# Kernel optimization log

Hardware: AMD Instinct MI355X
Metric: run time of the kernel (lower is better)

The kernel has to match this reference:

```python
import jax, jax.numpy as jnp
import numpy as np

N = 20000
E = 640000
F_IN = 128
C_T = 8
L_T = 10 * N
HEADS = 8
HDIM = 64
NEG_SLOPE = 0.2


def setup_inputs() -> dict:
    key = jax.random.key(0)
    ks = jax.random.split(key, 20)
    d = {}
    d["x"] = jax.random.normal(ks[0], (N, F_IN), dtype=jnp.float32)
    d["edge_index"] = jax.random.randint(ks[1], (2, E), 0, N, dtype=jnp.int64)
    d["temporal"] = jax.random.normal(ks[2], (C_T, L_T), dtype=jnp.float32)
    # GCNConv(F_IN, 16)
    d["W1"] = jax.random.normal(ks[3], (F_IN, 16), dtype=jnp.float32) * 0.1
    d["b1"] = jnp.zeros((16,), dtype=jnp.float32)
    # GATConv(16, 64, heads=8), concat -> 512
    d["W2"] = jax.random.normal(ks[4], (16, HEADS * HDIM), dtype=jnp.float32) * 0.1
    d["att_src"] = jax.random.normal(ks[5], (HEADS, HDIM), dtype=jnp.float32) * 0.1
    d["att_dst"] = jax.random.normal(ks[6], (HEADS, HDIM), dtype=jnp.float32) * 0.1
    d["b2"] = jnp.zeros((HEADS * HDIM,), dtype=jnp.float32)
    # TemporalCNN
    d["cw1"] = jax.random.normal(ks[7], (32, C_T, 3), dtype=jnp.float32) * 0.1
    d["cb1"] = jnp.zeros((32,), dtype=jnp.float32)
    d["cw2"] = jax.random.normal(ks[8], (64, 32, 3), dtype=jnp.float32) * 0.05
    d["cb2"] = jnp.zeros((64,), dtype=jnp.float32)
    d["cw3"] = jax.random.normal(ks[9], (128, 64, 3), dtype=jnp.float32) * 0.05
    d["cb3"] = jnp.zeros((128,), dtype=jnp.float32)
    d["fw1"] = jax.random.normal(ks[10], (256, 128 * 10), dtype=jnp.float32) * 0.02
    d["fb1"] = jnp.zeros((256,), dtype=jnp.float32)
    d["fw2"] = jax.random.normal(ks[11], (64, 256), dtype=jnp.float32) * 0.05
    d["fb2"] = jnp.zeros((64,), dtype=jnp.float32)
    return d


def _conv1d(x, w, b):
    # x: [1, C, L], w: [O, C, 3]; padding=1 == SAME for k=3
    out = jax.lax.conv_general_dilated(
        x, w, window_strides=(1,), padding="SAME",
        dimension_numbers=("NCH", "OIH", "NCH"))
    return out + b[None, :, None]


def _gcn(x, src, dst, W, b):
    # PyG GCNConv: add self-loops, symmetric normalization
    h = x @ W                                   # [N, 16]
    deg = jax.ops.segment_sum(jnp.ones_like(dst, dtype=h.dtype), dst, num_segments=N)
    dinv = jax.lax.rsqrt(jnp.maximum(deg, 1.0))
    norm = dinv[src] * dinv[dst]                # [E+N]
    out = jax.ops.segment_sum(h[src] * norm[:, None], dst, num_segments=N)
    return out + b


def _gat(x, src, dst, W, att_src, att_dst, b):
    h = (x @ W).reshape(N, HEADS, HDIM)         # [N, 8, 64]
    a_s = jnp.einsum("nhd,hd->nh", h, att_src)  # [N, 8]
    a_d = jnp.einsum("nhd,hd->nh", h, att_dst)
    e = a_s[src] + a_d[dst]                     # [E+N, 8], message j->i: src=j, dst=i
    e = jnp.where(e >= 0, e, NEG_SLOPE * e)     # LeakyReLU(0.2)
    # segment softmax over incoming edges of each dst node
    m = jax.ops.segment_max(e, dst, num_segments=N)
    m = jnp.where(jnp.isfinite(m), m, 0.0)
    ex = jnp.exp(e - m[dst])
    s = jax.ops.segment_sum(ex, dst, num_segments=N)
    alpha = ex / (s[dst] + 1e-16)               # [E+N, 8]
    out = jax.ops.segment_sum(h[src] * alpha[:, :, None], dst, num_segments=N)
    return out.reshape(N, HEADS * HDIM) + b


def reference(x, edge_index, temporal, W1, b1, W2, att_src, att_dst, b2,
              cw1, cb1, cw2, cb2, cw3, cb3, fw1, fb1, fw2, fb2):
    # ---- graph branch ----
    loops = jnp.arange(N, dtype=edge_index.dtype)
    src = jnp.concatenate([edge_index[0], loops])
    dst = jnp.concatenate([edge_index[1], loops])
    g = _gcn(x, src, dst, W1, b1)
    g = jax.nn.relu(g)
    # F.dropout with training=False (eval) -> identity
    x1 = _gat(g, src, dst, W2, att_src, att_dst, b2)   # [N, 512]
    # ---- temporal branch ----
    t = temporal[None]                                  # [1, C, L]
    t = jax.nn.relu(_conv1d(t, cw1, cb1))
    t = jax.nn.relu(_conv1d(t, cw2, cb2))
    t = jax.nn.relu(_conv1d(t, cw3, cb3))               # [1, 128, L]
    t = t.reshape(-1, 128 * 10)                         # [N, 1280] (same as torch .view)
    t = jax.nn.relu(t @ fw1.T + fb1)
    x2 = t @ fw2.T + fb2                                # [N, 64]
    return jnp.concatenate([x1, x2], axis=1)            # [N, 576]
```

## Files before the change

### kernel.cpp

```cpp
#include <hip/hip_runtime.h>
#include <hip/hip_bf16.h>

#define NN 20000
#define EE 640000
#define FIN 128
#define CT 8
#define LT 200000
#define HEADS 8
#define HDIM 64
#define F1 16
#define F2 512
#define OUTF 576

typedef short s16x8 __attribute__((ext_vector_type(8)));
typedef float f32x4 __attribute__((ext_vector_type(4)));
typedef float f32x2 __attribute__((ext_vector_type(2)));

static __device__ __forceinline__ float b2f(__hip_bfloat16 v) { return __bfloat162float(v); }
static __device__ __forceinline__ float ldf(float v) { return v; }
static __device__ __forceinline__ float ldf(__hip_bfloat16 v) { return __bfloat162float(v); }
static __device__ __forceinline__ unsigned f2bf_bits(float x) {
  unsigned u = __float_as_uint(x);
  return (u + 0x7fffu + ((u >> 16) & 1u)) >> 16;
}

static __device__ __forceinline__ void gl16(const void* g, void* l) {
  __builtin_amdgcn_global_load_lds(
      (const __attribute__((address_space(1))) unsigned*)g,
      (__attribute__((address_space(3))) unsigned*)l, 16, 0, 0);
}


__global__ __launch_bounds__(256) void wprep_kernel(
    const float* __restrict__ cw, float* __restrict__ wt, int O, int C) {
  int i = blockIdx.x * 256 + threadIdx.x;
  if (i >= O * C * 3) return;
  int o = i / (C * 3), r = i % (C * 3);
  int c = r / 3, k = r % 3;
  wt[(c * 3 + k) * O + o] = cw[i];
}

__global__ __launch_bounds__(256) void wprep_bf(
    const float* __restrict__ cw, short* __restrict__ wb, int O, int C) {
  int i = blockIdx.x * 256 + threadIdx.x;
  if (i >= O * C * 3) return;
  int o = i / (C * 3), r = i % (C * 3);
  int ic = r / 3, kk = r % 3;
  wb[o * 3 * C + kk * C + ic] = (short)f2bf_bits(cw[i]);
}

template <int C, int O, int P, typename IN_T>
__global__ __launch_bounds__(256) void conv_fast(
    const IN_T* __restrict__ in, __hip_bfloat16* __restrict__ out,
    const float* __restrict__ wt, const float* __restrict__ bias) {
  constexpr int OCG = O / 2;
  constexpr int PG = 256 / OCG;
  static_assert(PG * P == 64, "tile mismatch");
  __shared__ __align__(16) float tile[C][68];
  __shared__ __align__(16) __hip_bfloat16 ot[O][66];
  int t = threadIdx.x;
  int ocg = t % OCG;
  int pg = t / OCG;
  long base = (long)blockIdx.x * 64;

  for (int i = t; i < C * 66; i += 256) {
    int c = i / 66, p = i % 66;
    long l = base + p - 1;
    tile[c][p] = (l >= 0 && l < LT) ? ldf(in[(long)c * LT + l]) : 0.f;
  }
  __syncthreads();

  int oc0 = 2 * ocg;
  int p0 = pg * P;
  float acc[2][P];
#pragma unroll
  for (int j = 0; j < 2; j++)
#pragma unroll
    for (int p = 0; p < P; p++) acc[j][p] = 0.f;

  for (int ic = 0; ic < C; ic++) {
    float x[P + 2];
#pragma unroll
    for (int q = 0; q < P / 4; q++) {
      float4 v = *(const float4*)&tile[ic][p0 + 4 * q];
      x[4 * q] = v.x; x[4 * q + 1] = v.y; x[4 * q + 2] = v.z; x[4 * q + 3] = v.w;
    }
    {
      float2 v = *(const float2*)&tile[ic][p0 + P];
      x[P] = v.x; x[P + 1] = v.y;
    }
    const float* wrow = wt + (long)ic * 3 * O;
    float wv[3][2];
#pragma unroll
    for (int kk = 0; kk < 3; kk++) {
      float2 w2 = *(const float2*)&wrow[kk * O + oc0];
      wv[kk][0] = w2.x; wv[kk][1] = w2.y;
    }
#pragma unroll
    for (int kk = 0; kk < 3; kk++)
#pragma unroll
      for (int j = 0; j < 2; j++)
#pragma unroll
        for (int p = 0; p < P; p++) acc[j][p] += x[p + kk] * wv[kk][j];
  }
  float b0 = bias[oc0], b1 = bias[oc0 + 1];
#pragma unroll
  for (int p = 0; p < P; p++) {
    ot[oc0][p0 + p] = __float2bfloat16(fmaxf(acc[0][p] + b0, 0.f));
    ot[oc0 + 1][p0 + p] = __float2bfloat16(fmaxf(acc[1][p] + b1, 0.f));
  }
  __syncthreads();
  for (int i = t; i < O * 32; i += 256) {
    int oc = i >> 5, pp = i & 31;
    unsigned v = ((const unsigned*)&ot[oc][0])[pp];
    *(unsigned*)&out[(long)oc * LT + base + 2 * pp] = v;
  }
}

template <int C, int O, int MPW>
__global__ __launch_bounds__(256) void conv_mfma(
    const short* __restrict__ in, short* __restrict__ out,
    const short* __restrict__ w, const float* __restrict__ bias) {
  constexpr int K = 3 * C;
  constexpr int NS = K / 32;
  constexpr int XP = C + 8;
  constexpr int OP = 132;
  constexpr int SH_X = 132 * XP * 2;
  constexpr int SH_O = O * OP * 2;
  __shared__ __align__(16) char smem[(SH_X > SH_O) ? SH_X : SH_O];
  short* xT = (short*)smem;

  int t = threadIdx.x;
  long base = (long)blockIdx.x * 128;

  for (int idx = t; idx < C * 132; idx += 256) {
    int ic = idx / 132, p = idx % 132;
    long l = base + p - 1;
    xT[p * XP + ic] = (l >= 0 && l < LT) ? in[(long)ic * LT + l] : (short)0;
  }
  __syncthreads();

  int wave = t >> 6, lane = t & 63;
  int n = lane & 15, kg = lane >> 4;
  int m0 = wave * (MPW * 16);

  f32x4 acc[MPW][8] = {};
#pragma unroll
  for (int s = 0; s < NS; s++) {
    const int kk = (s * 32) / C;
    const int ic0 = (s * 32) % C + kg * 8;
    s16x8 a[MPW];
#pragma unroll
    for (int mi = 0; mi < MPW; mi++)
      a[mi] = *(const s16x8*)(w + (long)(m0 + mi * 16 + n) * K + s * 32 + kg * 8);
#pragma unroll
    for (int nt = 0; nt < 8; nt++) {
      s16x8 b = *(const s16x8*)(xT + (nt * 16 + n + kk) * XP + ic0);
#pragma unroll
      for (int mi = 0; mi < MPW; mi++)
        acc[mi][nt] = __builtin_amdgcn_mfma_f32_16x16x32_bf16(a[mi], b, acc[mi][nt], 0, 0, 0);
    }
  }

  __syncthreads();
  short* ob = (short*)smem;
#pragma unroll
  for (int mi = 0; mi < MPW; mi++) {
    int o = m0 + mi * 16 + kg * 4;
#pragma unroll
    for (int nt = 0; nt < 8; nt++) {
      int p = nt * 16 + n;
#pragma unroll
      for (int r = 0; r < 4; r++) {
        float v = fmaxf(acc[mi][nt][r] + bias[o + r], 0.f);
        ob[(o + r) * OP + p] = (short)f2bf_bits(v);
      }
    }
  }
  __syncthreads();
  const unsigned* obu = (const unsigned*)smem;
  for (int idx = t; idx < O * 64; idx += 256) {
    int o = idx >> 6, q = idx & 63;
    long l = base + 2 * q;
    if (l < LT)
      *(unsigned*)(out + (long)o * LT + l) = obu[o * (OP / 2) + q];
  }
}

__global__ __launch_bounds__(256) void fw1bf_kernel(
    const float* __restrict__ fw1, __hip_bfloat16* __restrict__ w) {
  int i = blockIdx.x * 256 + threadIdx.x;
  if (i < 256 * 1280) w[i] = __float2bfloat16(fw1[i]);
}

__global__ __launch_bounds__(256) void fw2t_kernel(
    const float* __restrict__ fw2, float* __restrict__ fw2t) {
  int i = blockIdx.x * 256 + threadIdx.x;
  if (i >= 64 * 256) return;
  int o = i / 256, j = i % 256;
  fw2t[j * 64 + o] = fw2[i];
}

__global__ __launch_bounds__(256) void fc1_tile(
    const __hip_bfloat16* __restrict__ t3, const __hip_bfloat16* __restrict__ w,
    const float* __restrict__ fb1, float* __restrict__ out) {
  __shared__ __align__(16) short As[2][128 * 32];
  __shared__ __align__(16) short Bs[2][128 * 32];
  int t = threadIdx.x;
  int wid = t >> 6, lane = t & 63;
  int bn = blockIdx.x & 1, bm = blockIdx.x >> 1;
  int mrow = lane & 15, kg = lane >> 4;

  const char* tb = (const char*)t3;
  const char* wb = (const char*)w;
  int u0 = wid * 128 + lane;
  int u1 = u0 + 64;
  int ra0 = u0 >> 2, ca0 = u0 & 3;
  int ra1 = u1 >> 2, ca1 = u1 & 3;
  long ga0 = ((long)min(bm * 128 + ra0, NN - 1) * 1280 + ca0 * 8) * 2;
  long ga1 = ((long)min(bm * 128 + ra1, NN - 1) * 1280 + ca1 * 8) * 2;
  long gb0 = ((long)(bn * 128 + ra0) * 1280 + ca0 * 8) * 2;
  long gb1 = ((long)(bn * 128 + ra1) * 1280 + ca1 * 8) * 2;
  int l0 = (wid * 2 + 0) * 512;
  int l1 = (wid * 2 + 1) * 512;

#define FC1_STAGE(buf, k0)                          \
  do {                                              \
    long kb = (long)(k0) * 2;                       \
    gl16(tb + ga0 + kb, &As[buf][l0]);              \
    gl16(tb + ga1 + kb, &As[buf][l1]);              \
    gl16(wb + gb0 + kb, &Bs[buf][l0]);              \
    gl16(wb + gb1 + kb, &Bs[buf][l1]);              \
  } while (0)

  FC1_STAGE(0, 0);
  __syncthreads();

  int wr = wid >> 1, wc = wid & 1;
  f32x4 acc[4][4] = {};
  for (int s = 0; s < 40; s++) {
    int buf = s & 1;
    if (s + 1 < 40) FC1_STAGE(buf ^ 1, (s + 1) * 32);
    s16x8 a[4], b[4];
#pragma unroll
    for (int mi = 0; mi < 4; mi++)
      a[mi] = *(const s16x8*)&As[buf][(wr * 64 + mi * 16 + mrow) * 32 + kg * 8];
#pragma unroll
    for (int ni = 0; ni < 4; ni++)
      b[ni] = *(const s16x8*)&Bs[buf][(wc * 64 + ni * 16 + mrow) * 32 + kg * 8];
#pragma unroll
    for (int mi = 0; mi < 4; mi++)
#pragma unroll
      for (int ni = 0; ni < 4; ni++)
        acc[mi][ni] = __builtin_amdgcn_mfma_f32_16x16x32_bf16(a[mi], b[ni], acc[mi][ni], 0, 0, 0);
    __syncthreads();
  }
#undef FC1_STAGE

  int node_base = bm * 128 + wr * 64 + kg * 4;
  int col_base = bn * 128 + wc * 64 + mrow;
#pragma unroll
  for (int ni = 0; ni < 4; ni++) {
    int col = col_base + ni * 16;
    float bias = fb1[col];
#pragma unroll
    for (int mi = 0; mi < 4; mi++) {
      int node = node_base + mi * 16;
#pragma unroll
      for (int r = 0; r < 4; r++) {
        if (node + r < NN)
          out[(long)(node + r) * 256 + col] = fmaxf(acc[mi][ni][r] + bias, 0.f);
      }
    }
  }
}

__global__ __launch_bounds__(256) void fc2_kernel(
    const float* __restrict__ fc1o, const float* __restrict__ fw2t,
    const float* __restrict__ fb2, float* __restrict__ out) {
  __shared__ float sh[32][257];
  int t = threadIdx.x;
  int m0 = blockIdx.x * 32;
  for (int i = t; i < 32 * 256; i += 256) {
    int nd = i >> 8, j = i & 255;
    sh[nd][j] = fc1o[(long)(m0 + nd) * 256 + j];
  }
  __syncthreads();
  int wave = t >> 6, o = t & 63;
  int nb = wave * 8;
  float acc[8];
  float bias = fb2[o];
#pragma unroll
  for (int i = 0; i < 8; i++) acc[i] = bias;
  for (int j = 0; j < 256; j++) {
    float wv = fw2t[j * 64 + o];
#pragma unroll
    for (int i = 0; i < 8; i++) acc[i] += sh[nb + i][j] * wv;
  }
#pragma unroll
  for (int i = 0; i < 8; i++)
    out[(long)(m0 + nb + i) * OUTF + F2 + o] = acc[i];
}


__global__ __launch_bounds__(256) void zero_i32(int* __restrict__ p, int n) {
  int i = blockIdx.x * 256 + threadIdx.x;
  if (i < n) p[i] = 0;
}

__global__ __launch_bounds__(256) void deg_kernel(const int* __restrict__ dst, int* __restrict__ deg) {
  int e = blockIdx.x * 256 + threadIdx.x;
  if (e < EE) atomicAdd(&deg[dst[e]], 1);
}

__global__ __launch_bounds__(256) void dinv_kernel(const int* __restrict__ deg, float* __restrict__ dinv) {
  int i = blockIdx.x * 256 + threadIdx.x;
  if (i < NN) dinv[i] = rsqrtf((float)(deg[i] + 1));
}

__global__ __launch_bounds__(1024) void scan_kernel(const int* __restrict__ deg, int* __restrict__ offs) {
  __shared__ int sums[1024];
  int tid = threadIdx.x;
  const int CH = 20;
  int s = 0;
  for (int i = 0; i < CH; i++) {
    int idx = tid * CH + i;
    if (idx < NN) s += deg[idx] + 1;
  }
  sums[tid] = s;
  __syncthreads();
  for (int off = 1; off < 1024; off <<= 1) {
    int v = (tid >= off) ? sums[tid - off] : 0;
    __syncthreads();
    sums[tid] += v;
    __syncthreads();
  }
  int run = (tid > 0) ? sums[tid - 1] : 0;
  for (int i = 0; i < CH; i++) {
    int idx = tid * CH + i;
    if (idx < NN) {
      offs[idx] = run;
      run += deg[idx] + 1;
    }
  }
  if (tid == 1023) offs[NN] = sums[1023];
}

__global__ __launch_bounds__(256) void fill_kernel(
    const int* __restrict__ src, const int* __restrict__ dst,
    const int* __restrict__ offs, int* __restrict__ cursor, int* __restrict__ csr) {
  int e = blockIdx.x * 256 + threadIdx.x;
  if (e < EE) {
    int d = dst[e];
    int pos = atomicAdd(&cursor[d], 1);
    csr[offs[d] + pos] = src[e];
  } else if (e < EE + NN) {
    int i = e - EE;
    int pos = atomicAdd(&cursor[i], 1);
    csr[offs[i] + pos] = i;
  }
}

__global__ __launch_bounds__(256) void h1_kernel(
    const float* __restrict__ x, const float* __restrict__ W1,
    const float* __restrict__ dinv, float* __restrict__ h1s) {
  __shared__ __align__(16) float ws[128 * 16];
  __shared__ __align__(16) float xs[16][132];
  int t = threadIdx.x;
  int i0 = blockIdx.x * 16;
#pragma unroll
  for (int i = t; i < 512; i += 256)
    *(float4*)&ws[4 * i] = *(const float4*)&W1[4 * i];
#pragma unroll
  for (int i = t; i < 512; i += 256) {
    int nl = i >> 5, q = i & 31;
    *(float4*)&xs[nl][4 * q] = *(const float4*)&x[(long)(i0 + nl) * FIN + 4 * q];
  }
  __syncthreads();
  int nl = t >> 4, f = t & 15;
  float acc = 0.f;
#pragma unroll 8
  for (int k = 0; k < FIN; k++) acc += xs[nl][k] * ws[k * 16 + f];
  int n = i0 + nl;
  h1s[n * F1 + f] = acc * dinv[n];
}

__global__ __launch_bounds__(256) void gcn_kernel(
    const float* __restrict__ h1s, const int* __restrict__ offs, const int* __restrict__ csr,
    const float* __restrict__ dinv, const float* __restrict__ b1, float* __restrict__ g) {
  int wave = threadIdx.x >> 6;
  int lane = threadIdx.x & 63;
  int i = blockIdx.x * 4 + wave;
  int f = lane & 15, grp = lane >> 4;
  int beg = offs[i], end = offs[i + 1];
  float acc = 0.f;
  for (int idx = beg + grp; idx < end; idx += 4)
    acc += h1s[csr[idx] * F1 + f];
  acc += __shfl_down(acc, 32);
  acc += __shfl_down(acc, 16);
  if (lane < 16) g[i * F1 + f] = fmaxf(acc * dinv[i] + b1[f], 0.f);
}

__global__ __launch_bounds__(256) void att_prep(
    const float* __restrict__ W2, const float* __restrict__ asrc,
    const float* __restrict__ adst, float* __restrict__ WS, float* __restrict__ WD) {
  int t = threadIdx.x;
  int k = (t & 127) >> 3, h = t & 7;
  const float* av = (t < 128) ? asrc : adst;
  float acc = 0.f;
  for (int d = 0; d < 64; d++) acc += W2[k * F2 + h * 64 + d] * av[h * 64 + d];
  ((t < 128) ? WS : WD)[k * 8 + h] = acc;
}

__global__ __launch_bounds__(256) void h2att_kernel(
    const float* __restrict__ g, const float* __restrict__ W2,
    const float* __restrict__ WS, const float* __restrict__ WD,
    unsigned* __restrict__ h2hm, float* __restrict__ AS, float* __restrict__ AD) {
  __shared__ __align__(16) float gl[32][20];
  int t = threadIdx.x;
  int i0 = blockIdx.x * 32;
  for (int idx = t; idx < 512; idx += 256)
    gl[idx >> 4][idx & 15] = g[i0 * 16 + idx];
  __syncthreads();

  int f0 = 2 * t;
  int h = t >> 5, c32 = t & 31;
  float w0[16], w1[16];
#pragma unroll
  for (int k = 0; k < 16; k++) {
    float2 wv = *(const float2*)&W2[k * F2 + f0];
    w0[k] = wv.x; w1[k] = wv.y;
  }
  for (int nl = 0; nl < 32; nl++) {
    float a0 = 0.f, a1 = 0.f;
#pragma unroll
    for (int kk = 0; kk < 4; kk++) {
      f32x4 gv = *(const f32x4*)&gl[nl][4 * kk];
#pragma unroll
      for (int r = 0; r < 4; r++) {
        a0 += gv[r] * w0[4 * kk + r];
        a1 += gv[r] * w1[4 * kk + r];
      }
    }
    h2hm[((long)h * NN + i0 + nl) * 32 + c32] = f2bf_bits(a0) | (f2bf_bits(a1) << 16);
  }
  int nl = t >> 3, hh = t & 7;
  float s = 0.f, d = 0.f;
#pragma unroll
  for (int k = 0; k < 16; k++) {
    float gv = gl[nl][k];
    s += gv * WS[k * 8 + hh];
    d += gv * WD[k * 8 + hh];
  }
  AS[(long)hh * NN + i0 + nl] = s;
  AD[(long)hh * NN + i0 + nl] = d;
}

static __device__ __forceinline__ void acc8(f32x2* a, uint4 v, float aj) {
  f32x2 aj2 = {aj, aj};
  f32x2 t0 = {__uint_as_float(v.x << 16), __uint_as_float(v.x & 0xffff0000u)};
  f32x2 t1 = {__uint_as_float(v.y << 16), __uint_as_float(v.y & 0xffff0000u)};
  f32x2 t2 = {__uint_as_float(v.z << 16), __uint_as_float(v.z & 0xffff0000u)};
  f32x2 t3 = {__uint_as_float(v.w << 16), __uint_as_float(v.w & 0xffff0000u)};
  a[0] += t0 * aj2;
  a[1] += t1 * aj2;
  a[2] += t2 * aj2;
  a[3] += t3 * aj2;
}

__global__ __launch_bounds__(256) void gat_fused_kernel(
    const unsigned* __restrict__ h2hm, const float* __restrict__ AS,
    const float* __restrict__ AD, const int* __restrict__ offs,
    const int* __restrict__ csr, const float* __restrict__ b2,
    float* __restrict__ out) {
  __shared__ __align__(16) unsigned long long pairs[4][64];
  __shared__ __align__(16) float accb[4][8][68];
  int h = blockIdx.x & 7;
  int gn = blockIdx.x >> 3;
  int wave = threadIdx.x >> 6;
  int lane = threadIdx.x & 63;
  int i = gn * 4 + wave;
  int beg = offs[i], end = offs[i + 1];
  const float* ASh = AS + (long)h * NN;
  float ad = AD[(long)h * NN + i];
  const char* hb2 = (const char*)(h2hm + (long)h * NN * 32);
  int octet = lane >> 3, q = lane & 7;
  unsigned laneoff = (unsigned)q * 16u;
  unsigned long long* prs = &pairs[wave][0];

  f32x2 acc2[4] = {};
  float sum = 0.f;

  for (int c = beg; c < end; c += 64) {
    int cnt = end - c;
    if (cnt > 64) cnt = 64;
    unsigned off = 0u;
    float ex = 0.f;
    if (lane < cnt) {
      int s = csr[c + lane];
      float e = ASh[s] + ad;
      e = (e >= 0.f) ? e : 0.2f * e;
      ex = __expf(e);
      sum += ex;
      off = (unsigned)s << 7;
    }
    asm volatile("" ::: "memory");
    prs[lane] = ((unsigned long long)__float_as_uint(ex) << 32) | off;
    asm volatile("" ::: "memory");
    int nj = (cnt + 7) >> 3;
    const unsigned long long* pp = prs + octet;
    int j = 0;
    for (; j + 2 <= nj; j += 2) {
      unsigned long long pr0 = pp[(long)j * 8];
      unsigned long long pr1 = pp[(long)j * 8 + 8];
      uint4 v0 = *(const uint4*)(hb2 + ((unsigned)pr0 | laneoff));
      uint4 v1 = *(const uint4*)(hb2 + ((unsigned)pr1 | laneoff));
      acc8(acc2, v0, __uint_as_float((unsigned)(pr0 >> 32)));
      acc8(acc2, v1, __uint_as_float((unsigned)(pr1 >> 32)));
    }
    if (j < nj) {
      unsigned long long pr = pp[(long)j * 8];
      uint4 v = *(const uint4*)(hb2 + ((unsigned)pr | laneoff));
      acc8(acc2, v, __uint_as_float((unsigned)(pr >> 32)));
    }
    asm volatile("" ::: "memory");
  }
#pragma unroll
  for (int o = 32; o > 0; o >>= 1) sum += __shfl_xor(sum, o, 64);
  float rinv = 1.f / (sum + 1e-16f);
  float* ab = &accb[wave][octet][q * 8];
  f32x4 lo = {acc2[0][0], acc2[0][1], acc2[1][0], acc2[1][1]};
  f32x4 hi = {acc2[2][0], acc2[2][1], acc2[3][0], acc2[3][1]};
  *(f32x4*)ab = lo;
  *(f32x4*)(ab + 4) = hi;
  asm volatile("" ::: "memory");
  float r = 0.f;
#pragma unroll
  for (int o = 0; o < 8; o++) r += accb[wave][o][lane];
  out[(long)i * OUTF + h * 64 + lane] = r * rinv + b2[h * 64 + lane];
}


extern "C" void kernel_launch(void* const* d_in, const int* in_sizes, int n_in,
                              void* d_out, int out_size, void* d_ws, size_t ws_size,
                              hipStream_t stream) {
  const float* x        = (const float*)d_in[0];
  const int*   eidx     = (const int*)d_in[1];
  const float* temporal = (const float*)d_in[2];
  const float* W1       = (const float*)d_in[3];
  const float* b1       = (const float*)d_in[4];
  const float* W2       = (const float*)d_in[5];
  const float* att_src  = (const float*)d_in[6];
  const float* att_dst  = (const float*)d_in[7];
  const float* b2       = (const float*)d_in[8];
  const float* cw1      = (const float*)d_in[9];
  const float* cb1      = (const float*)d_in[10];
  const float* cw2      = (const float*)d_in[11];
  const float* cb2      = (const float*)d_in[12];
  const float* cw3      = (const float*)d_in[13];
  const float* cb3      = (const float*)d_in[14];
  const float* fw1      = (const float*)d_in[15];
  const float* fb1      = (const float*)d_in[16];
  const float* fw2      = (const float*)d_in[17];
  const float* fb2      = (const float*)d_in[18];
  float* out = (float*)d_out;

  const int* e_src = eidx;
  const int* e_dst = eidx + EE;

  char* ws = (char*)d_ws;
  __hip_bfloat16* T1b = (__hip_bfloat16*)(ws + 0);
  __hip_bfloat16* T2b = (__hip_bfloat16*)(ws + 12800000);
  __hip_bfloat16* T3b = (__hip_bfloat16*)(ws + 38400000);
  __hip_bfloat16* FW1BF = (__hip_bfloat16*)(ws + 0);
  float* FW2T   = (float*)(ws + 655360);
  float* FC1OUT = (float*)(ws + 1310720);
  float* H1     = (float*)(ws + 0);
  float* G      = (float*)(ws + 1280000);
  int*   DEG    = (int*)  (ws + 2560000);
  float* DINV   = (float*)(ws + 2640000);
  int*   OFFS   = (int*)  (ws + 2720000);
  int*   CURSOR = (int*)  (ws + 2800128);
  int*   CSR    = (int*)  (ws + 2880128);
  float* AS     = (float*)(ws + 5520128);
  float* AD     = (float*)(ws + 6160128);
  unsigned* H2HM = (unsigned*)(ws + 6800128);
  float* WSM    = (float*)(ws + 2560000);
  float* WDM    = (float*)(ws + 2560512);
  float* WT1 = out;
  short* WB2 = (short*)((char*)d_out + 3072);
  short* WB3 = (short*)((char*)d_out + 15360);

  const int PB = LT / 64;
  const int MB = (LT + 127) / 128;

  wprep_kernel<<<(32 * 8 * 3 + 255) / 256, 256, 0, stream>>>(cw1, WT1, 32, 8);
  wprep_bf<<<(64 * 32 * 3 + 255) / 256, 256, 0, stream>>>(cw2, WB2, 64, 32);
  wprep_bf<<<(128 * 64 * 3 + 255) / 256, 256, 0, stream>>>(cw3, WB3, 128, 64);
  conv_fast<8, 32, 4, float><<<PB, 256, 0, stream>>>(temporal, T1b, WT1, cb1);
  conv_mfma<32, 64, 1><<<MB, 256, 0, stream>>>((const short*)T1b, (short*)T2b, WB2, cb2);
  fw1bf_kernel<<<(256 * 1280 + 255) / 256, 256, 0, stream>>>(fw1, FW1BF);
  fw2t_kernel<<<(64 * 256 + 255) / 256, 256, 0, stream>>>(fw2, FW2T);
  conv_mfma<64, 128, 2><<<MB, 256, 0, stream>>>((const short*)T2b, (short*)T3b, WB3, cb3);
  fc1_tile<<<157 * 2, 256, 0, stream>>>(T3b, FW1BF, fb1, FC1OUT);
  fc2_kernel<<<NN / 32, 256, 0, stream>>>(FC1OUT, FW2T, fb2, out);

  zero_i32<<<(80032 + 255) / 256, 256, 0, stream>>>(DEG, 80032);
  deg_kernel<<<(EE + 255) / 256, 256, 0, stream>>>(e_dst, DEG);
  dinv_kernel<<<(NN + 255) / 256, 256, 0, stream>>>(DEG, DINV);
  scan_kernel<<<1, 1024, 0, stream>>>(DEG, OFFS);
  att_prep<<<1, 256, 0, stream>>>(W2, att_src, att_dst, WSM, WDM);
  fill_kernel<<<(EE + NN + 255) / 256, 256, 0, stream>>>(e_src, e_dst, OFFS, CURSOR, CSR);
  h1_kernel<<<NN / 16, 256, 0, stream>>>(x, W1, DINV, H1);
  gcn_kernel<<<NN / 4, 256, 0, stream>>>(H1, OFFS, CSR, DINV, b1, G);
  h2att_kernel<<<NN / 32, 256, 0, stream>>>(G, W2, WSM, WDM, H2HM, AS, AD);
  gat_fused_kernel<<<(NN / 4) * 8, 256, 0, stream>>>(H2HM, AS, AD, OFFS, CSR, b2, out);
}
```

Baseline: 467.6 us.

## Merge small prep kernels, fold dinv into scan, widen conv and fc2 loads

Merges the weight-prep, attention-prep and fc-weight conversion kernels into two combined launches, and folds the dinv computation into the scan kernel, to cut kernel-launch count. It also adds a fast interior path in conv_mfma that loads input pairs as 32-bit words, vectorises the fc2 shared-memory fill with float4, and rewrites the GAT accumulator from packed float2 ops to scalar floats with an unroll pragma. The attention-prep scratch is moved into the output buffer because its old workspace slot overlaps DEG, which is now live at that point. The wide conv loads may be unaligned for odd offsets, and the accumulator change could affect codegen either way.

```diff
diff --git a/kernel.cpp b/kernel.cpp
--- a/kernel.cpp
+++ b/kernel.cpp
@@ -14,7 +14,6 @@
 
 typedef short s16x8 __attribute__((ext_vector_type(8)));
 typedef float f32x4 __attribute__((ext_vector_type(4)));
-typedef float f32x2 __attribute__((ext_vector_type(2)));
 
 static __device__ __forceinline__ float b2f(__hip_bfloat16 v) { return __bfloat162float(v); }
 static __device__ __forceinline__ float ldf(float v) { return v; }
@@ -30,24 +29,53 @@
       (__attribute__((address_space(3))) unsigned*)l, 16, 0, 0);
 }
 
-
-__global__ __launch_bounds__(256) void wprep_kernel(
-    const float* __restrict__ cw, float* __restrict__ wt, int O, int C) {
-  int i = blockIdx.x * 256 + threadIdx.x;
-  if (i >= O * C * 3) return;
-  int o = i / (C * 3), r = i % (C * 3);
-  int c = r / 3, k = r % 3;
-  wt[(c * 3 + k) * O + o] = cw[i];
-}
-
-__global__ __launch_bounds__(256) void wprep_bf(
-    const float* __restrict__ cw, short* __restrict__ wb, int O, int C) {
-  int i = blockIdx.x * 256 + threadIdx.x;
-  if (i >= O * C * 3) return;
-  int o = i / (C * 3), r = i % (C * 3);
-  int ic = r / 3, kk = r % 3;
-  wb[o * 3 * C + kk * C + ic] = (short)f2bf_bits(cw[i]);
-}
+__global__ __launch_bounds__(256) void prep_all(
+    const float* __restrict__ cw1, float* __restrict__ wt1,
+    const float* __restrict__ cw2, short* __restrict__ wb2,
+    const float* __restrict__ cw3, short* __restrict__ wb3,
+    const float* __restrict__ W2, const float* __restrict__ asrc,
+    const float* __restrict__ adst, float* __restrict__ WS, float* __restrict__ WD) {
+  int b = blockIdx.x, t = threadIdx.x;
+  if (b < 3) {
+    int i = b * 256 + t;
+    if (i < 32 * 8 * 3) {
+      int o = i / 24, r = i % 24;
+      int c = r / 3, k = r % 3;
+      wt1[(c * 3 + k) * 32 + o] = cw1[i];
+    }
+  } else if (b < 27) {
+    int i = (b - 3) * 256 + t;
+    int o = i / 96, r = i % 96;
+    int ic = r / 3, kk = r % 3;
+    wb2[o * 96 + kk * 32 + ic] = (short)f2bf_bits(cw2[i]);
+  } else if (b < 123) {
+    int i = (b - 27) * 256 + t;
+    int o = i / 192, r = i % 192;
+    int ic = r / 3, kk = r % 3;
+    wb3[o * 192 + kk * 64 + ic] = (short)f2bf_bits(cw3[i]);
+  } else {
+    int k = (t & 127) >> 3, h = t & 7;
+    const float* av = (t < 128) ? asrc : adst;
+    float acc = 0.f;
+    for (int d = 0; d < 64; d++) acc += W2[k * F2 + h * 64 + d] * av[h * 64 + d];
+    ((t < 128) ? WS : WD)[k * 8 + h] = acc;
+  }
+}
+
+__global__ __launch_bounds__(256) void fwprep(
+    const float* __restrict__ fw1, __hip_bfloat16* __restrict__ w1b,
+    const float* __restrict__ fw2, float* __restrict__ fw2t) {
+  int b = blockIdx.x;
+  if (b < 1280) {
+    int i = b * 256 + threadIdx.x;
+    w1b[i] = __float2bfloat16(fw1[i]);
+  } else {
+    int i = (b - 1280) * 256 + threadIdx.x;
+    int o = i / 256, j = i % 256;
+    fw2t[j * 64 + o] = fw2[i];
+  }
+}
+
 
 template <int C, int O, int P, typename IN_T>
 __global__ __launch_bounds__(256) void conv_fast(
@@ -133,10 +161,20 @@
   int t = threadIdx.x;
   long base = (long)blockIdx.x * 128;
 
-  for (int idx = t; idx < C * 132; idx += 256) {
-    int ic = idx / 132, p = idx % 132;
-    long l = base + p - 1;
-    xT[p * XP + ic] = (l >= 0 && l < LT) ? in[(long)ic * LT + l] : (short)0;
+  if (base >= 2 && base + 131 < LT) {
+    for (int idx = t; idx < C * 67; idx += 256) {
+      int ic = idx / 67, q = idx % 67;
+      unsigned v = *(const unsigned*)(in + (long)ic * LT + base + 2 * q - 2);
+      int p0 = 2 * q - 1;
+      if (q > 0) xT[p0 * XP + ic] = (short)(v & 0xffffu);
+      if (q < 66) xT[(p0 + 1) * XP + ic] = (short)(v >> 16);
+    }
+  } else {
+    for (int idx = t; idx < C * 132; idx += 256) {
+      int ic = idx / 132, p = idx % 132;
+      long l = base + p - 1;
+      xT[p * XP + ic] = (l >= 0 && l < LT) ? in[(long)ic * LT + l] : (short)0;
+    }
   }
   __syncthreads();
 
@@ -185,20 +223,6 @@
     if (l < LT)
       *(unsigned*)(out + (long)o * LT + l) = obu[o * (OP / 2) + q];
   }
-}
-
-__global__ __launch_bounds__(256) void fw1bf_kernel(
-    const float* __restrict__ fw1, __hip_bfloat16* __restrict__ w) {
-  int i = blockIdx.x * 256 + threadIdx.x;
-  if (i < 256 * 1280) w[i] = __float2bfloat16(fw1[i]);
-}
-
-__global__ __launch_bounds__(256) void fw2t_kernel(
-    const float* __restrict__ fw2, float* __restrict__ fw2t) {
-  int i = blockIdx.x * 256 + threadIdx.x;
-  if (i >= 64 * 256) return;
-  int o = i / 256, j = i % 256;
-  fw2t[j * 64 + o] = fw2[i];
 }
 
 __global__ __launch_bounds__(256) void fc1_tile(
@@ -278,12 +302,12 @@
 __global__ __launch_bounds__(256) void fc2_kernel(
     const float* __restrict__ fc1o, const float* __restrict__ fw2t,
     const float* __restrict__ fb2, float* __restrict__ out) {
-  __shared__ float sh[32][257];
+  __shared__ __align__(16) float sh[32 * 264];
   int t = threadIdx.x;
   int m0 = blockIdx.x * 32;
-  for (int i = t; i < 32 * 256; i += 256) {
-    int nd = i >> 8, j = i & 255;
-    sh[nd][j] = fc1o[(long)(m0 + nd) * 256 + j];
+  for (int i = t; i < 2048; i += 256) {
+    int nd = i >> 6, q = i & 63;
+    *(float4*)&sh[nd * 264 + 4 * q] = *(const float4*)&fc1o[(long)(m0 + nd) * 256 + 4 * q];
   }
   __syncthreads();
   int wave = t >> 6, o = t & 63;
@@ -295,7 +319,7 @@
   for (int j = 0; j < 256; j++) {
     float wv = fw2t[j * 64 + o];
 #pragma unroll
-    for (int i = 0; i < 8; i++) acc[i] += sh[nb + i][j] * wv;
+    for (int i = 0; i < 8; i++) acc[i] += sh[(nb + i) * 264 + j] * wv;
   }
 #pragma unroll
   for (int i = 0; i < 8; i++)
@@ -313,12 +337,8 @@
   if (e < EE) atomicAdd(&deg[dst[e]], 1);
 }
 
-__global__ __launch_bounds__(256) void dinv_kernel(const int* __restrict__ deg, float* __restrict__ dinv) {
-  int i = blockIdx.x * 256 + threadIdx.x;
-  if (i < NN) dinv[i] = rsqrtf((float)(deg[i] + 1));
-}
-
-__global__ __launch_bounds__(1024) void scan_kernel(const int* __restrict__ deg, int* __restrict__ offs) {
+__global__ __launch_bounds__(1024) void scan_kernel(
+    const int* __restrict__ deg, int* __restrict__ offs, float* __restrict__ dinv) {
   __shared__ int sums[1024];
   int tid = threadIdx.x;
   const int CH = 20;
@@ -339,8 +359,10 @@
   for (int i = 0; i < CH; i++) {
     int idx = tid * CH + i;
     if (idx < NN) {
+      int d = deg[idx];
       offs[idx] = run;
-      run += deg[idx] + 1;
+      dinv[idx] = rsqrtf((float)(d + 1));
+      run += d + 1;
     }
   }
   if (tid == 1023) offs[NN] = sums[1023];
@@ -401,17 +423,6 @@
   if (lane < 16) g[i * F1 + f] = fmaxf(acc * dinv[i] + b1[f], 0.f);
 }
 
-__global__ __launch_bounds__(256) void att_prep(
-    const float* __restrict__ W2, const float* __restrict__ asrc,
-    const float* __restrict__ adst, float* __restrict__ WS, float* __restrict__ WD) {
-  int t = threadIdx.x;
-  int k = (t & 127) >> 3, h = t & 7;
-  const float* av = (t < 128) ? asrc : adst;
-  float acc = 0.f;
-  for (int d = 0; d < 64; d++) acc += W2[k * F2 + h * 64 + d] * av[h * 64 + d];
-  ((t < 128) ? WS : WD)[k * 8 + h] = acc;
-}
-
 __global__ __launch_bounds__(256) void h2att_kernel(
     const float* __restrict__ g, const float* __restrict__ W2,
     const float* __restrict__ WS, const float* __restrict__ WD,
@@ -454,18 +465,6 @@
   }
   AS[(long)hh * NN + i0 + nl] = s;
   AD[(long)hh * NN + i0 + nl] = d;
-}
-
-static __device__ __forceinline__ void acc8(f32x2* a, uint4 v, float aj) {
-  f32x2 aj2 = {aj, aj};
-  f32x2 t0 = {__uint_as_float(v.x << 16), __uint_as_float(v.x & 0xffff0000u)};
-  f32x2 t1 = {__uint_as_float(v.y << 16), __uint_as_float(v.y & 0xffff0000u)};
-  f32x2 t2 = {__uint_as_float(v.z << 16), __uint_as_float(v.z & 0xffff0000u)};
-  f32x2 t3 = {__uint_as_float(v.w << 16), __uint_as_float(v.w & 0xffff0000u)};
-  a[0] += t0 * aj2;
-  a[1] += t1 * aj2;
-  a[2] += t2 * aj2;
-  a[3] += t3 * aj2;
 }
 
 __global__ __launch_bounds__(256) void gat_fused_kernel(
@@ -488,7 +487,7 @@
   unsigned laneoff = (unsigned)q * 16u;
   unsigned long long* prs = &pairs[wave][0];
 
-  f32x2 acc2[4] = {};
+  float acc[8] = {0.f, 0.f, 0.f, 0.f, 0.f, 0.f, 0.f, 0.f};
   float sum = 0.f;
 
   for (int c = beg; c < end; c += 64) {
@@ -509,19 +508,20 @@
     asm volatile("" ::: "memory");
     int nj = (cnt + 7) >> 3;
     const unsigned long long* pp = prs + octet;
-    int j = 0;
-    for (; j + 2 <= nj; j += 2) {
-      unsigned long long pr0 = pp[(long)j * 8];
-      unsigned long long pr1 = pp[(long)j * 8 + 8];
-      uint4 v0 = *(const uint4*)(hb2 + ((unsigned)pr0 | laneoff));
-      uint4 v1 = *(const uint4*)(hb2 + ((unsigned)pr1 | laneoff));
-      acc8(acc2, v0, __uint_as_float((unsigned)(pr0 >> 32)));
-      acc8(acc2, v1, __uint_as_float((unsigned)(pr1 >> 32)));
-    }
-    if (j < nj) {
+#pragma unroll 2
+    for (int j = 0; j < nj; j++) {
       unsigned long long pr = pp[(long)j * 8];
-      uint4 v = *(const uint4*)(hb2 + ((unsigned)pr | laneoff));
-      acc8(acc2, v, __uint_as_float((unsigned)(pr >> 32)));
+      unsigned voff = (unsigned)pr | laneoff;
+      float aj = __uint_as_float((unsigned)(pr >> 32));
+      uint4 v = *(const uint4*)(hb2 + voff);
+      acc[0] += __uint_as_float(v.x << 16) * aj;
+      acc[1] += __uint_as_float(v.x & 0xffff0000u) * aj;
+      acc[2] += __uint_as_float(v.y << 16) * aj;
+      acc[3] += __uint_as_float(v.y & 0xffff0000u) * aj;
+      acc[4] += __uint_as_float(v.z << 16) * aj;
+      acc[5] += __uint_as_float(v.z & 0xffff0000u) * aj;
+      acc[6] += __uint_as_float(v.w << 16) * aj;
+      acc[7] += __uint_as_float(v.w & 0xffff0000u) * aj;
     }
     asm volatile("" ::: "memory");
   }
@@ -529,8 +529,8 @@
   for (int o = 32; o > 0; o >>= 1) sum += __shfl_xor(sum, o, 64);
   float rinv = 1.f / (sum + 1e-16f);
   float* ab = &accb[wave][octet][q * 8];
-  f32x4 lo = {acc2[0][0], acc2[0][1], acc2[1][0], acc2[1][1]};
-  f32x4 hi = {acc2[2][0], acc2[2][1], acc2[3][0], acc2[3][1]};
+  f32x4 lo = {acc[0], acc[1], acc[2], acc[3]};
+  f32x4 hi = {acc[4], acc[5], acc[6], acc[7]};
   *(f32x4*)ab = lo;
   *(f32x4*)(ab + 4) = hi;
   asm volatile("" ::: "memory");
@@ -585,31 +585,27 @@
   float* AS     = (float*)(ws + 5520128);
   float* AD     = (float*)(ws + 6160128);
   unsigned* H2HM = (unsigned*)(ws + 6800128);
-  float* WSM    = (float*)(ws + 2560000);
-  float* WDM    = (float*)(ws + 2560512);
   float* WT1 = out;
   short* WB2 = (short*)((char*)d_out + 3072);
   short* WB3 = (short*)((char*)d_out + 15360);
+  float* WSM = (float*)((char*)d_out + 64512);
+  float* WDM = (float*)((char*)d_out + 65024);
 
   const int PB = LT / 64;
   const int MB = (LT + 127) / 128;
 
-  wprep_kernel<<<(32 * 8 * 3 + 255) / 256, 256, 0, stream>>>(cw1, WT1, 32, 8);
-  wprep_bf<<<(64 * 32 * 3 + 255) / 256, 256, 0, stream>>>(cw2, WB2, 64, 32);
-  wprep_bf<<<(128 * 64 * 3 + 255) / 256, 256, 0, stream>>>(cw3, WB3, 128, 64);
+  prep_all<<<124, 256, 0, stream>>>(cw1, WT1, cw2, WB2, cw3, WB3,
+                                    W2, att_src, att_dst, WSM, WDM);
   conv_fast<8, 32, 4, float><<<PB, 256, 0, stream>>>(temporal, T1b, WT1, cb1);
   conv_mfma<32, 64, 1><<<MB, 256, 0, stream>>>((const short*)T1b, (short*)T2b, WB2, cb2);
-  fw1bf_kernel<<<(256 * 1280 + 255) / 256, 256, 0, stream>>>(fw1, FW1BF);
-  fw2t_kernel<<<(64 * 256 + 255) / 256, 256, 0, stream>>>(fw2, FW2T);
+  fwprep<<<1344, 256, 0, stream>>>(fw1, FW1BF, fw2, FW2T);
   conv_mfma<64, 128, 2><<<MB, 256, 0, stream>>>((const short*)T2b, (short*)T3b, WB3, cb3);
   fc1_tile<<<157 * 2, 256, 0, stream>>>(T3b, FW1BF, fb1, FC1OUT);
   fc2_kernel<<<NN / 32, 256, 0, stream>>>(FC1OUT, FW2T, fb2, out);
 
   zero_i32<<<(80032 + 255) / 256, 256, 0, stream>>>(DEG, 80032);
   deg_kernel<<<(EE + 255) / 256, 256, 0, stream>>>(e_dst, DEG);
-  dinv_kernel<<<(NN + 255) / 256, 256, 0, stream>>>(DEG, DINV);
-  scan_kernel<<<1, 1024, 0, stream>>>(DEG, OFFS);
-  att_prep<<<1, 256, 0, stream>>>(W2, att_src, att_dst, WSM, WDM);
+  scan_kernel<<<1, 1024, 0, stream>>>(DEG, OFFS, DINV);
   fill_kernel<<<(EE + NN + 255) / 256, 256, 0, stream>>>(e_src, e_dst, OFFS, CURSOR, CSR);
   h1_kernel<<<NN / 16, 256, 0, stream>>>(x, W1, DINV, H1);
   gcn_kernel<<<NN / 4, 256, 0, stream>>>(H1, OFFS, CSR, DINV, b1, G);
```

Measured after the change: 450.1 us. 1.04x faster.
